# Kernel optimization log

Hardware: AMD Instinct MI355X
Metric: run time of the kernel (lower is better)

Reference implementation:

```python
import jax, jax.numpy as jnp
import numpy as np

E = 512    # len_embeddings
T = 32     # tokennum
H = 256    # hidden_unit
IT = 5     # ICI iterations
B = 4096   # batch
EPS = 1e-6


def setup_inputs() -> dict:
    key = jax.random.key(0)
    k0, k1, k2, k3, k4 = jax.random.split(key, 5)
    x = jax.random.normal(k0, (B, E), dtype=jnp.float32)
    glorot = np.sqrt(2.0 / (E + H)).astype(np.float32)
    w_in = jax.random.normal(k1, (T, E, H), dtype=jnp.float32) * glorot
    w_val = jax.random.normal(k2, (T, E, H), dtype=jnp.float32) * glorot
    # alphas: per-token, per-iteration inhibition strengths (trained; sample nonzero)
    alphas = jax.random.uniform(k3, (T, IT), dtype=jnp.float32) * 0.5
    # scales: per-token output scale (init 1.0, perturb slightly)
    scales = 1.0 + 0.1 * jax.random.normal(k4, (T, H), dtype=jnp.float32)
    gamma = jnp.ones((T, H), dtype=jnp.float32)
    beta = jnp.zeros((T, H), dtype=jnp.float32)
    return {"x": x, "w_in": w_in, "w_val": w_val, "alphas": alphas,
            "scales": scales, "gamma": gamma, "beta": beta}


def reference(x, w_in, w_val, alphas, scales, gamma, beta):
    # batched per-token projection: [B,E] x [T,E,H] -> [B,T,H]
    hidden = jnp.einsum('be,teh->bth', x, w_in)
    # iterative competitive inhibition (fixed small IT loop)
    x_t = jax.nn.relu(hidden)
    for i in range(alphas.shape[1]):
        m = jnp.mean(x_t, axis=-1, keepdims=True)          # [B,T,1]
        a = alphas[:, i][None, :, None]                     # [1,T,1]
        x_t = jax.nn.relu(x_t - a * m)
    sparse_g = scales[None] * x_t                           # [B,T,H]
    # gated value path
    value = jnp.einsum('be,teh->bth', x, w_val)
    s = sparse_g * value
    # per-token LayerNorm over hidden dim, eps=1e-6
    mu = jnp.mean(s, axis=-1, keepdims=True)
    var = jnp.mean((s - mu) ** 2, axis=-1, keepdims=True)
    out = (s - mu) / jnp.sqrt(var + EPS) * gamma[None] + beta[None]
    return out  # [B, T, H]
```

## Files before the change

### kernel.cpp

```cpp
#include <hip/hip_runtime.h>
#include <cstdint>

using u16 = unsigned short;
using u32 = unsigned int;

constexpr int kB  = 4096;
constexpr int kE  = 512;
constexpr int kT  = 32;
constexpr int kH  = 256;
constexpr int kIT = 5;
constexpr float kEPS = 1e-6f;

typedef __attribute__((ext_vector_type(8)))  short short8;
typedef __attribute__((ext_vector_type(16))) float floatx16;
typedef __attribute__((ext_vector_type(8)))  u16   ushort8;
typedef __attribute__((ext_vector_type(4)))  float floatv4;

__device__ __forceinline__ u16 f2bf(float f) {
  u32 u = __builtin_bit_cast(u32, f);
  return (u16)((u + 0x7fffu + ((u >> 16) & 1u)) >> 16);
}

__device__ __forceinline__ floatx16 mfma32(short8 a, short8 b, floatx16 c) {
  return __builtin_amdgcn_mfma_f32_32x32x16_bf16(a, b, c, 0, 0, 0);
}

__device__ __forceinline__ void ntstore4(float* p, float4 v) {
  __builtin_nontemporal_store(__builtin_bit_cast(floatv4, v), (floatv4*)p);
}

__global__ __launch_bounds__(256) void pack_x_kernel(
    const float* __restrict__ x, u16* __restrict__ xp) {
  __shared__ __attribute__((aligned(16))) float tile[64 * 132];
  const int slab = blockIdx.x >> 2;
  const int kg   = blockIdx.x & 3;
  const int tid  = threadIdx.x;

  const int r0 = tid >> 5;
  const int c0 = (tid & 31) * 4;
#pragma unroll
  for (int p = 0; p < 8; ++p) {
    const int r = p * 8 + r0;
    const float4 v = *(const float4*)(x + (size_t)(slab * 64 + r) * kE + kg * 128 + c0);
    *(float4*)(tile + r * 132 + c0) = v;
  }
  __syncthreads();

  const int wv = tid >> 6, lane = tid & 63;
#pragma unroll
  for (int q = 0; q < 4; ++q) {
    const int cc   = wv * 4 + q;
    const int ks_l = cc >> 1;
    const int mt   = cc & 1;
    const int rl   = mt * 32 + (lane & 31);
    const int kl   = ks_l * 16 + (lane >> 5) * 8;
    const float4 f0 = *(const float4*)(tile + rl * 132 + kl);
    const float4 f1 = *(const float4*)(tile + rl * 132 + kl + 4);
    ushort8 o;
    o[0] = f2bf(f0.x); o[1] = f2bf(f0.y); o[2] = f2bf(f0.z); o[3] = f2bf(f0.w);
    o[4] = f2bf(f1.x); o[5] = f2bf(f1.y); o[6] = f2bf(f1.z); o[7] = f2bf(f1.w);
    const int c = slab * 64 + (kg * 8 + ks_l) * 2 + mt;
    *(ushort8*)(xp + (size_t)c * 512 + lane * 8) = o;
  }
}

__global__ __launch_bounds__(256) void pack_w_kernel(
    const float* __restrict__ w_in, const float* __restrict__ w_val,
    u16* __restrict__ wp) {
  __shared__ __attribute__((aligned(16))) float tile[64 * 68];
  const int wb   = blockIdx.x;
  const int tl   = wb & 31;
  const int et   = tl >> 2;
  const int ht   = tl & 3;
  const int tm   = wb >> 5;
  const int t    = tm >> 1, mat = tm & 1;
  const int tid  = threadIdx.x;
  const float* src = (mat ? w_val : w_in) + (size_t)t * kE * kH +
                     (size_t)(et * 64) * kH + ht * 64;
  const int lrow = tid >> 4, lc4 = (tid & 15) * 4;
#pragma unroll
  for (int p = 0; p < 4; ++p) {
    const int e = lrow + p * 16;
    const float4 v = *(const float4*)(src + (size_t)e * kH + lc4);
    tile[e * 68 + lc4 + 0] = v.x; tile[e * 68 + lc4 + 1] = v.y;
    tile[e * 68 + lc4 + 2] = v.z; tile[e * 68 + lc4 + 3] = v.w;
  }
  __syncthreads();
  const int ks_l = tid >> 6, lane = tid & 63;
  const int kloc = ks_l * 16 + (lane >> 5) * 8;
#pragma unroll
  for (int nt_l = 0; nt_l < 2; ++nt_l) {
    const int nloc = nt_l * 32 + (lane & 31);
    ushort8 o;
#pragma unroll
    for (int j = 0; j < 8; ++j) o[j] = f2bf(tile[(kloc + j) * 68 + nloc]);
    const int c = t * 512 + (et * 4 + ks_l) * 16 + (ht * 2 + nt_l) * 2 + mat;
    *(ushort8*)(wp + (size_t)c * 512 + lane * 8) = o;
  }
}

__global__ __launch_bounds__(256, 2) void fused_kernel(
    const u16* __restrict__ xp, const u16* __restrict__ wp,
    const float* __restrict__ alphas, const float* __restrict__ scales,
    const float* __restrict__ gamma, const float* __restrict__ beta,
    float* __restrict__ out) {
  __shared__ __attribute__((aligned(16))) float sAcc[32 * 256];

  const int tid  = threadIdx.x;
  const int wv   = tid >> 6;
  const int lane = tid & 63;
  const int l31  = lane & 31;
  const int h    = lane >> 5;

  const int bid  = blockIdx.x;
  const int xcd  = bid & 7;
  const int r_   = bid >> 3;
  const int st   = r_ >> 6;
  const int wi   = r_ & 63;
  const int t    = xcd * 4 + (wi >> 4);
  const int slab = st * 16 + (wi & 15);

  const u16* xpb = xp + (size_t)slab * (32 * 2 * 512) + lane * 8;
  const u16* wpb = wp + (size_t)t * (32 * 16 * 512) + (size_t)(wv * 2) * 1024 + lane * 8;

  floatx16 ai[2][2], av[2][2];
#pragma unroll
  for (int m = 0; m < 2; ++m)
#pragma unroll
    for (int n = 0; n < 2; ++n) { ai[m][n] = (floatx16)0.f; av[m][n] = (floatx16)0.f; }

  short8 A[3][2], BI[3][2], BV[3][2];
#pragma unroll
  for (int p = 0; p < 2; ++p) {
    A[p][0]  = *(const short8*)(xpb + p * 1024);
    A[p][1]  = *(const short8*)(xpb + p * 1024 + 512);
    BI[p][0] = *(const short8*)(wpb + p * 8192);
    BV[p][0] = *(const short8*)(wpb + p * 8192 + 512);
    BI[p][1] = *(const short8*)(wpb + p * 8192 + 1024);
    BV[p][1] = *(const short8*)(wpb + p * 8192 + 1536);
  }

#pragma unroll
  for (int ks = 0; ks < 32; ++ks) {
    const int cur = ks % 3;
    const int nx  = (ks + 2) % 3;
    const int kn  = (ks < 30) ? ks + 2 : 31;
    A[nx][0]  = *(const short8*)(xpb + kn * 1024);
    A[nx][1]  = *(const short8*)(xpb + kn * 1024 + 512);
    BI[nx][0] = *(const short8*)(wpb + kn * 8192);
    BV[nx][0] = *(const short8*)(wpb + kn * 8192 + 512);
    BI[nx][1] = *(const short8*)(wpb + kn * 8192 + 1024);
    BV[nx][1] = *(const short8*)(wpb + kn * 8192 + 1536);
    ai[0][0] = mfma32(A[cur][0], BI[cur][0], ai[0][0]);
    ai[1][0] = mfma32(A[cur][1], BI[cur][0], ai[1][0]);
    ai[0][1] = mfma32(A[cur][0], BI[cur][1], ai[0][1]);
    ai[1][1] = mfma32(A[cur][1], BI[cur][1], ai[1][1]);
    av[0][0] = mfma32(A[cur][0], BV[cur][0], av[0][0]);
    av[1][0] = mfma32(A[cur][1], BV[cur][0], av[1][0]);
    av[0][1] = mfma32(A[cur][0], BV[cur][1], av[0][1]);
    av[1][1] = mfma32(A[cur][1], BV[cur][1], av[1][1]);
  }

  const float inv_h = 1.0f / kH;
  float al[kIT];
#pragma unroll
  for (int i = 0; i < kIT; ++i) al[i] = alphas[t * kIT + i] * inv_h;

  const int row_r = tid >> 3;
  const int seg   = tid & 7;
  const int r4    = (row_r & 7) << 2;

#pragma unroll
  for (int mt = 0; mt < 2; ++mt) {
    __syncthreads();
#pragma unroll
    for (int nt = 0; nt < 2; ++nt)
#pragma unroll
      for (int q = 0; q < 16; ++q) {
        const int r   = (q & 3) + 8 * (q >> 2) + 4 * h;
        const int col = wv * 64 + nt * 32 + l31;
        sAcc[r * 256 + (col ^ ((r & 7) << 2))] = ai[mt][nt][q];
      }
    __syncthreads();

    float4 xt[8];
#pragma unroll
    for (int j = 0; j < 8; ++j) {
      xt[j] = *(const float4*)(sAcc + row_r * 256 + seg * 32 + ((4 * j) ^ r4));
#pragma unroll
      for (int i = 0; i < 4; ++i) xt[j][i] = fmaxf(xt[j][i], 0.f);
    }

#pragma unroll
    for (int it = 0; it < kIT; ++it) {
      float4 s4 = xt[0];
#pragma unroll
      for (int j = 1; j < 8; ++j) s4 += xt[j];
      float v = s4.x + s4.y + s4.z + s4.w;
      v += __shfl_xor(v, 1, 8);
      v += __shfl_xor(v, 2, 8);
      v += __shfl_xor(v, 4, 8);
      const float m = al[it] * v;
#pragma unroll
      for (int j = 0; j < 8; ++j)
#pragma unroll
        for (int i = 0; i < 4; ++i) xt[j][i] = fmaxf(xt[j][i] - m, 0.f);
    }

    __syncthreads();
#pragma unroll
    for (int nt = 0; nt < 2; ++nt)
#pragma unroll
      for (int q = 0; q < 16; ++q) {
        const int r   = (q & 3) + 8 * (q >> 2) + 4 * h;
        const int col = wv * 64 + nt * 32 + l31;
        sAcc[r * 256 + (col ^ ((r & 7) << 2))] = av[mt][nt][q];
      }
    __syncthreads();

    float4 res[8];
    float sum = 0.f, ssq = 0.f;
#pragma unroll
    for (int j = 0; j < 8; ++j) {
      const int cb = seg * 32 + ((4 * j) ^ r4);
      const int lc = seg * 32 + 4 * j;
      const float4 a4 = *(const float4*)(sAcc + row_r * 256 + cb);
      const float4 sc = *(const float4*)(scales + t * kH + lc);
      float4 s;
#pragma unroll
      for (int i = 0; i < 4; ++i) {
        s[i] = sc[i] * xt[j][i] * a4[i];
        sum += s[i];
        ssq += s[i] * s[i];
      }
      res[j] = s;
    }
    sum += __shfl_xor(sum, 1, 8);  ssq += __shfl_xor(ssq, 1, 8);
    sum += __shfl_xor(sum, 2, 8);  ssq += __shfl_xor(ssq, 2, 8);
    sum += __shfl_xor(sum, 4, 8);  ssq += __shfl_xor(ssq, 4, 8);
    const float mu  = sum * inv_h;
    const float var = ssq * inv_h - mu * mu;
    const float rs  = rsqrtf(var + kEPS);

#pragma unroll
    for (int j = 0; j < 8; ++j) {
      const int cb = seg * 32 + ((4 * j) ^ r4);
      const int lc = seg * 32 + 4 * j;
      const float4 g4 = *(const float4*)(gamma + t * kH + lc);
      const float4 b4 = *(const float4*)(beta + t * kH + lc);
      float4 o;
#pragma unroll
      for (int i = 0; i < 4; ++i) o[i] = (res[j][i] - mu) * rs * g4[i] + b4[i];
      *(float4*)(sAcc + row_r * 256 + cb) = o;
    }
    __syncthreads();

#pragma unroll
    for (int r8 = 0; r8 < 8; ++r8) {
      const int rr = wv * 8 + r8;
      const int rb = (rr & 7) << 2;
      const float4 v = *(const float4*)(sAcc + rr * 256 + ((4 * lane) ^ rb));
      ntstore4(out + (size_t)(slab * 64 + mt * 32 + rr) * (kT * kH) + t * kH + 4 * lane, v);
    }
  }
}

extern "C" void kernel_launch(void* const* d_in, const int* in_sizes, int n_in,
                              void* d_out, int out_size, void* d_ws, size_t ws_size,
                              hipStream_t stream) {
  const float* x      = (const float*)d_in[0];
  const float* w_in   = (const float*)d_in[1];
  const float* w_val  = (const float*)d_in[2];
  const float* alphas = (const float*)d_in[3];
  const float* scales = (const float*)d_in[4];
  const float* gamma  = (const float*)d_in[5];
  const float* beta   = (const float*)d_in[6];
  float* out = (float*)d_out;

  u16* xp = (u16*)d_ws;
  u16* wp = xp + (size_t)64 * 32 * 2 * 512;

  pack_x_kernel<<<256, 256, 0, stream>>>(x, xp);
  pack_w_kernel<<<2048, 256, 0, stream>>>(w_in, w_val, wp);
  fused_kernel<<<kT * (kB / 64), 256, 0, stream>>>(xp, wp, alphas, scales,
                                                   gamma, beta, out);
}
```

Before: 346.6 us.

## Stage weight tiles through LDS with async global_load_lds double buffering

Replaces the per-wave direct global register loads of the packed weight fragments with asynchronous global-to-LDS copies. The copies are double-buffered across 16 K-steps of two sub-steps each, and each step ends in a block barrier. Each wave copies a quarter of the tile and all waves then read their fragments from LDS, while x fragments stay in registers and are double-buffered. This aims to cut per-wave global load latency and register-pipelined vector loads. In exchange it adds LDS traffic, 16 barriers, and reuses the accumulator smem region as the weight buffer.

```diff
diff --git a/kernel.cpp b/kernel.cpp
--- a/kernel.cpp
+++ b/kernel.cpp
@@ -27,6 +27,12 @@
 
 __device__ __forceinline__ void ntstore4(float* p, float4 v) {
   __builtin_nontemporal_store(__builtin_bit_cast(floatv4, v), (floatv4*)p);
+}
+
+__device__ __forceinline__ void gload16(const u16* gsrc, u16* ldst) {
+  __builtin_amdgcn_global_load_lds(
+      (const __attribute__((address_space(1))) u32*)gsrc,
+      (__attribute__((address_space(3))) u32*)ldst, 16, 0, 0);
 }
 
 __global__ __launch_bounds__(256) void pack_x_kernel(
@@ -104,7 +110,8 @@
     const float* __restrict__ alphas, const float* __restrict__ scales,
     const float* __restrict__ gamma, const float* __restrict__ beta,
     float* __restrict__ out) {
-  __shared__ __attribute__((aligned(16))) float sAcc[32 * 256];
+  __shared__ __attribute__((aligned(16))) u16 sB[2][16384];
+  float* sAcc = (float*)sB;
 
   const int tid  = threadIdx.x;
   const int wv   = tid >> 6;
@@ -121,7 +128,9 @@
   const int slab = st * 16 + (wi & 15);
 
   const u16* xpb = xp + (size_t)slab * (32 * 2 * 512) + lane * 8;
-  const u16* wpb = wp + (size_t)t * (32 * 16 * 512) + (size_t)(wv * 2) * 1024 + lane * 8;
+  const u16* wpt = wp + (size_t)t * (32 * 16 * 512);
+  const u16* wps = wpt + lane * 8;
+  const int  q0  = wv * 8;
 
   floatx16 ai[2][2], av[2][2];
 #pragma unroll
@@ -129,36 +138,52 @@
 #pragma unroll
     for (int n = 0; n < 2; ++n) { ai[m][n] = (floatx16)0.f; av[m][n] = (floatx16)0.f; }
 
-  short8 A[3][2], BI[3][2], BV[3][2];
-#pragma unroll
-  for (int p = 0; p < 2; ++p) {
-    A[p][0]  = *(const short8*)(xpb + p * 1024);
-    A[p][1]  = *(const short8*)(xpb + p * 1024 + 512);
-    BI[p][0] = *(const short8*)(wpb + p * 8192);
-    BV[p][0] = *(const short8*)(wpb + p * 8192 + 512);
-    BI[p][1] = *(const short8*)(wpb + p * 8192 + 1024);
-    BV[p][1] = *(const short8*)(wpb + p * 8192 + 1536);
-  }
-
-#pragma unroll
-  for (int ks = 0; ks < 32; ++ks) {
-    const int cur = ks % 3;
-    const int nx  = (ks + 2) % 3;
-    const int kn  = (ks < 30) ? ks + 2 : 31;
-    A[nx][0]  = *(const short8*)(xpb + kn * 1024);
-    A[nx][1]  = *(const short8*)(xpb + kn * 1024 + 512);
-    BI[nx][0] = *(const short8*)(wpb + kn * 8192);
-    BV[nx][0] = *(const short8*)(wpb + kn * 8192 + 512);
-    BI[nx][1] = *(const short8*)(wpb + kn * 8192 + 1024);
-    BV[nx][1] = *(const short8*)(wpb + kn * 8192 + 1536);
-    ai[0][0] = mfma32(A[cur][0], BI[cur][0], ai[0][0]);
-    ai[1][0] = mfma32(A[cur][1], BI[cur][0], ai[1][0]);
-    ai[0][1] = mfma32(A[cur][0], BI[cur][1], ai[0][1]);
-    ai[1][1] = mfma32(A[cur][1], BI[cur][1], ai[1][1]);
-    av[0][0] = mfma32(A[cur][0], BV[cur][0], av[0][0]);
-    av[1][0] = mfma32(A[cur][1], BV[cur][0], av[1][0]);
-    av[0][1] = mfma32(A[cur][0], BV[cur][1], av[0][1]);
-    av[1][1] = mfma32(A[cur][1], BV[cur][1], av[1][1]);
+  short8 A_[2][2][2];
+
+#pragma unroll
+  for (int j = 0; j < 8; ++j) {
+    const int q = q0 + j;
+    gload16(wps + (size_t)q * 512, (u16*)sB[0] + q * 512);
+  }
+#pragma unroll
+  for (int ksl = 0; ksl < 2; ++ksl)
+#pragma unroll
+    for (int m = 0; m < 2; ++m)
+      A_[0][ksl][m] = *(const short8*)(xpb + (ksl * 2 + m) * 512);
+  __syncthreads();
+
+#pragma unroll
+  for (int p = 0; p < 16; ++p) {
+    const int db = p & 1, nx = db ^ 1;
+    if (p < 15) {
+#pragma unroll
+      for (int j = 0; j < 8; ++j) {
+        const int q = q0 + j;
+        gload16(wps + (size_t)((p + 1) * 32 + q) * 512, (u16*)sB[nx] + q * 512);
+      }
+#pragma unroll
+      for (int ksl = 0; ksl < 2; ++ksl)
+#pragma unroll
+        for (int m = 0; m < 2; ++m)
+          A_[nx][ksl][m] = *(const short8*)(xpb + (((p + 1) * 2 + ksl) * 2 + m) * 512);
+    }
+    const u16* sBp = (const u16*)sB[db] + lane * 8;
+#pragma unroll
+    for (int ksl = 0; ksl < 2; ++ksl) {
+      const short8 BI0 = *(const short8*)(sBp + (ksl * 16 + (wv * 2 + 0) * 2 + 0) * 512);
+      const short8 BV0 = *(const short8*)(sBp + (ksl * 16 + (wv * 2 + 0) * 2 + 1) * 512);
+      const short8 BI1 = *(const short8*)(sBp + (ksl * 16 + (wv * 2 + 1) * 2 + 0) * 512);
+      const short8 BV1 = *(const short8*)(sBp + (ksl * 16 + (wv * 2 + 1) * 2 + 1) * 512);
+      ai[0][0] = mfma32(A_[db][ksl][0], BI0, ai[0][0]);
+      ai[1][0] = mfma32(A_[db][ksl][1], BI0, ai[1][0]);
+      ai[0][1] = mfma32(A_[db][ksl][0], BI1, ai[0][1]);
+      ai[1][1] = mfma32(A_[db][ksl][1], BI1, ai[1][1]);
+      av[0][0] = mfma32(A_[db][ksl][0], BV0, av[0][0]);
+      av[1][0] = mfma32(A_[db][ksl][1], BV0, av[1][0]);
+      av[0][1] = mfma32(A_[db][ksl][0], BV1, av[0][1]);
+      av[1][1] = mfma32(A_[db][ksl][1], BV1, av[1][1]);
+    }
+    __syncthreads();
   }
 
   const float inv_h = 1.0f / kH;
```

Result: faster. 315.8 us (-8.9%).

## Stream GEMM operands through per-wave LDS ring via global_load_lds

Applied to the files above, without the earlier changes.

The main K loop now loads A and B fragments straight into a per-wave three-slot LDS ring with direct-to-LDS global loads instead of holding a triple-buffered register pipeline. Each step waits on vmcnt, reads the fragments back from LDS, and raises wave priority around the MFMA group. This is meant to cut register pressure and keep more global loads in flight. The cost is an extra LDS round trip per step and hand-written waitcnt logic that must match the load count exactly. The LDS buffer is also reused as the epilogue accumulator scratch.

```diff
diff --git a/kernel.cpp b/kernel.cpp
--- a/kernel.cpp
+++ b/kernel.cpp
@@ -27,6 +27,12 @@
 
 __device__ __forceinline__ void ntstore4(float* p, float4 v) {
   __builtin_nontemporal_store(__builtin_bit_cast(floatv4, v), (floatv4*)p);
+}
+
+__device__ __forceinline__ void gload16(const u16* gsrc, u16* ldst) {
+  __builtin_amdgcn_global_load_lds(
+      (const __attribute__((address_space(1))) u32*)gsrc,
+      (__attribute__((address_space(3))) u32*)ldst, 16, 0, 0);
 }
 
 __global__ __launch_bounds__(256) void pack_x_kernel(
@@ -104,7 +110,8 @@
     const float* __restrict__ alphas, const float* __restrict__ scales,
     const float* __restrict__ gamma, const float* __restrict__ beta,
     float* __restrict__ out) {
-  __shared__ __attribute__((aligned(16))) float sAcc[32 * 256];
+  __shared__ __attribute__((aligned(16))) u16 ring[4][3][3072];
+  float* sAcc = (float*)ring;
 
   const int tid  = threadIdx.x;
   const int wv   = tid >> 6;
@@ -120,8 +127,9 @@
   const int t    = xcd * 4 + (wi >> 4);
   const int slab = st * 16 + (wi & 15);
 
-  const u16* xpb = xp + (size_t)slab * (32 * 2 * 512) + lane * 8;
-  const u16* wpb = wp + (size_t)t * (32 * 16 * 512) + (size_t)(wv * 2) * 1024 + lane * 8;
+  const u16* xsrc = xp + (size_t)slab * (32 * 2 * 512) + lane * 8;
+  const u16* bsrc = wp + (size_t)t * (32 * 16 * 512) + (wv * 4) * 512 + lane * 8;
+  u16* const ring_w = &ring[wv][0][0];
 
   floatx16 ai[2][2], av[2][2];
 #pragma unroll
@@ -129,36 +137,48 @@
 #pragma unroll
     for (int n = 0; n < 2; ++n) { ai[m][n] = (floatx16)0.f; av[m][n] = (floatx16)0.f; }
 
-  short8 A[3][2], BI[3][2], BV[3][2];
-#pragma unroll
-  for (int p = 0; p < 2; ++p) {
-    A[p][0]  = *(const short8*)(xpb + p * 1024);
-    A[p][1]  = *(const short8*)(xpb + p * 1024 + 512);
-    BI[p][0] = *(const short8*)(wpb + p * 8192);
-    BV[p][0] = *(const short8*)(wpb + p * 8192 + 512);
-    BI[p][1] = *(const short8*)(wpb + p * 8192 + 1024);
-    BV[p][1] = *(const short8*)(wpb + p * 8192 + 1536);
-  }
-
-#pragma unroll
-  for (int ks = 0; ks < 32; ++ks) {
-    const int cur = ks % 3;
-    const int nx  = (ks + 2) % 3;
-    const int kn  = (ks < 30) ? ks + 2 : 31;
-    A[nx][0]  = *(const short8*)(xpb + kn * 1024);
-    A[nx][1]  = *(const short8*)(xpb + kn * 1024 + 512);
-    BI[nx][0] = *(const short8*)(wpb + kn * 8192);
-    BV[nx][0] = *(const short8*)(wpb + kn * 8192 + 512);
-    BI[nx][1] = *(const short8*)(wpb + kn * 8192 + 1024);
-    BV[nx][1] = *(const short8*)(wpb + kn * 8192 + 1536);
-    ai[0][0] = mfma32(A[cur][0], BI[cur][0], ai[0][0]);
-    ai[1][0] = mfma32(A[cur][1], BI[cur][0], ai[1][0]);
-    ai[0][1] = mfma32(A[cur][0], BI[cur][1], ai[0][1]);
-    ai[1][1] = mfma32(A[cur][1], BI[cur][1], ai[1][1]);
-    av[0][0] = mfma32(A[cur][0], BV[cur][0], av[0][0]);
-    av[1][0] = mfma32(A[cur][1], BV[cur][0], av[1][0]);
-    av[0][1] = mfma32(A[cur][0], BV[cur][1], av[0][1]);
-    av[1][1] = mfma32(A[cur][1], BV[cur][1], av[1][1]);
+  auto issue = [&](int pb, int slot) {
+    u16* d = ring_w + slot * 3072;
+    const u16* a = xsrc + (size_t)pb * 1024;
+    const u16* b = bsrc + (size_t)pb * 8192;
+    gload16(a,        d);
+    gload16(a + 512,  d + 512);
+    gload16(b,        d + 1024);
+    gload16(b + 512,  d + 1536);
+    gload16(b + 1024, d + 2048);
+    gload16(b + 1536, d + 2560);
+  };
+
+  issue(0, 0);
+  issue(1, 1);
+
+#pragma unroll
+  for (int p = 0; p < 32; ++p) {
+    if (p < 31) { asm volatile("s_waitcnt vmcnt(6)" ::: "memory"); }
+    else        { asm volatile("s_waitcnt vmcnt(0)" ::: "memory"); }
+    __builtin_amdgcn_sched_barrier(0);
+    if (p < 30) issue(p + 2, (p + 2) % 3);
+
+    const u16* base = ring_w + (p % 3) * 3072 + lane * 8;
+    const short8 A0  = *(const short8*)(base);
+    const short8 A1  = *(const short8*)(base + 512);
+    const short8 BI0 = *(const short8*)(base + 1024);
+    const short8 BV0 = *(const short8*)(base + 1536);
+    const short8 BI1 = *(const short8*)(base + 2048);
+    const short8 BV1 = *(const short8*)(base + 2560);
+    asm volatile("s_waitcnt lgkmcnt(0)" ::: "memory");
+    __builtin_amdgcn_sched_barrier(0);
+
+    __builtin_amdgcn_s_setprio(1);
+    ai[0][0] = mfma32(A0, BI0, ai[0][0]);
+    ai[1][0] = mfma32(A1, BI0, ai[1][0]);
+    ai[0][1] = mfma32(A0, BI1, ai[0][1]);
+    ai[1][1] = mfma32(A1, BI1, ai[1][1]);
+    av[0][0] = mfma32(A0, BV0, av[0][0]);
+    av[1][0] = mfma32(A1, BV0, av[1][0]);
+    av[0][1] = mfma32(A0, BV1, av[0][1]);
+    av[1][1] = mfma32(A1, BV1, av[1][1]);
+    __builtin_amdgcn_s_setprio(0);
   }
 
   const float inv_h = 1.0f / kH;
```

Result: faster. 302.4 us (-12.7%).

## Split fused kernel across 8 waves with one N-tile each to raise occupancy

Applied to the files above, without the earlier changes.

The fused GEMM+inhibition+LayerNorm kernel now launches 512 threads per block. Each of the 8 waves owns one 32-column N tile instead of two, which halves the accumulator and operand registers per wave, and prefetch depth drops from a 3-stage to a 2-stage register ring. The epilogue is remapped so 16 threads share a row, with wider shuffle reductions. The intent is higher occupancy and latency hiding through more resident waves. In exchange, each wave reuses fewer A fragments, so global loads per MFMA rise and block-level synchronisation costs more.

```diff
diff --git a/kernel.cpp b/kernel.cpp
--- a/kernel.cpp
+++ b/kernel.cpp
@@ -99,7 +99,7 @@
   }
 }
 
-__global__ __launch_bounds__(256, 2) void fused_kernel(
+__global__ __launch_bounds__(512, 4) void fused_kernel(
     const u16* __restrict__ xp, const u16* __restrict__ wp,
     const float* __restrict__ alphas, const float* __restrict__ scales,
     const float* __restrict__ gamma, const float* __restrict__ beta,
@@ -120,45 +120,35 @@
   const int t    = xcd * 4 + (wi >> 4);
   const int slab = st * 16 + (wi & 15);
 
-  const u16* xpb = xp + (size_t)slab * (32 * 2 * 512) + lane * 8;
-  const u16* wpb = wp + (size_t)t * (32 * 16 * 512) + (size_t)(wv * 2) * 1024 + lane * 8;
-
-  floatx16 ai[2][2], av[2][2];
-#pragma unroll
-  for (int m = 0; m < 2; ++m)
-#pragma unroll
-    for (int n = 0; n < 2; ++n) { ai[m][n] = (floatx16)0.f; av[m][n] = (floatx16)0.f; }
-
-  short8 A[3][2], BI[3][2], BV[3][2];
-#pragma unroll
-  for (int p = 0; p < 2; ++p) {
-    A[p][0]  = *(const short8*)(xpb + p * 1024);
-    A[p][1]  = *(const short8*)(xpb + p * 1024 + 512);
-    BI[p][0] = *(const short8*)(wpb + p * 8192);
-    BV[p][0] = *(const short8*)(wpb + p * 8192 + 512);
-    BI[p][1] = *(const short8*)(wpb + p * 8192 + 1024);
-    BV[p][1] = *(const short8*)(wpb + p * 8192 + 1536);
-  }
-
-#pragma unroll
-  for (int ks = 0; ks < 32; ++ks) {
-    const int cur = ks % 3;
-    const int nx  = (ks + 2) % 3;
-    const int kn  = (ks < 30) ? ks + 2 : 31;
-    A[nx][0]  = *(const short8*)(xpb + kn * 1024);
-    A[nx][1]  = *(const short8*)(xpb + kn * 1024 + 512);
-    BI[nx][0] = *(const short8*)(wpb + kn * 8192);
-    BV[nx][0] = *(const short8*)(wpb + kn * 8192 + 512);
-    BI[nx][1] = *(const short8*)(wpb + kn * 8192 + 1024);
-    BV[nx][1] = *(const short8*)(wpb + kn * 8192 + 1536);
-    ai[0][0] = mfma32(A[cur][0], BI[cur][0], ai[0][0]);
-    ai[1][0] = mfma32(A[cur][1], BI[cur][0], ai[1][0]);
-    ai[0][1] = mfma32(A[cur][0], BI[cur][1], ai[0][1]);
-    ai[1][1] = mfma32(A[cur][1], BI[cur][1], ai[1][1]);
-    av[0][0] = mfma32(A[cur][0], BV[cur][0], av[0][0]);
-    av[1][0] = mfma32(A[cur][1], BV[cur][0], av[1][0]);
-    av[0][1] = mfma32(A[cur][0], BV[cur][1], av[0][1]);
-    av[1][1] = mfma32(A[cur][1], BV[cur][1], av[1][1]);
+  const u16* xsrc = xp + (size_t)slab * (32 * 2 * 512) + lane * 8;
+  const u16* bsrc = wp + (size_t)t * (32 * 16 * 512) + (size_t)(wv * 2) * 512 + lane * 8;
+
+  floatx16 ai[2], av[2];
+#pragma unroll
+  for (int m = 0; m < 2; ++m) { ai[m] = (floatx16)0.f; av[m] = (floatx16)0.f; }
+
+  short8 A0[2], A1[2], BI[2], BV[2];
+#pragma unroll
+  for (int pb = 0; pb < 2; ++pb) {
+    A0[pb] = *(const short8*)(xsrc + pb * 1024);
+    A1[pb] = *(const short8*)(xsrc + pb * 1024 + 512);
+    BI[pb] = *(const short8*)(bsrc + (size_t)pb * 8192);
+    BV[pb] = *(const short8*)(bsrc + (size_t)pb * 8192 + 512);
+  }
+
+#pragma unroll
+  for (int p = 0; p < 32; ++p) {
+    const int cur = p & 1;
+    ai[0] = mfma32(A0[cur], BI[cur], ai[0]);
+    ai[1] = mfma32(A1[cur], BI[cur], ai[1]);
+    av[0] = mfma32(A0[cur], BV[cur], av[0]);
+    av[1] = mfma32(A1[cur], BV[cur], av[1]);
+    if (p < 30) {
+      A0[cur] = *(const short8*)(xsrc + (p + 2) * 1024);
+      A1[cur] = *(const short8*)(xsrc + (p + 2) * 1024 + 512);
+      BI[cur] = *(const short8*)(bsrc + (size_t)(p + 2) * 8192);
+      BV[cur] = *(const short8*)(bsrc + (size_t)(p + 2) * 8192 + 512);
+    }
   }
 
   const float inv_h = 1.0f / kH;
@@ -166,27 +156,25 @@
 #pragma unroll
   for (int i = 0; i < kIT; ++i) al[i] = alphas[t * kIT + i] * inv_h;
 
-  const int row_r = tid >> 3;
-  const int seg   = tid & 7;
+  const int row_r = tid >> 4;
+  const int seg   = tid & 15;
   const int r4    = (row_r & 7) << 2;
 
 #pragma unroll
   for (int mt = 0; mt < 2; ++mt) {
     __syncthreads();
 #pragma unroll
-    for (int nt = 0; nt < 2; ++nt)
-#pragma unroll
-      for (int q = 0; q < 16; ++q) {
-        const int r   = (q & 3) + 8 * (q >> 2) + 4 * h;
-        const int col = wv * 64 + nt * 32 + l31;
-        sAcc[r * 256 + (col ^ ((r & 7) << 2))] = ai[mt][nt][q];
-      }
-    __syncthreads();
-
-    float4 xt[8];
-#pragma unroll
-    for (int j = 0; j < 8; ++j) {
-      xt[j] = *(const float4*)(sAcc + row_r * 256 + seg * 32 + ((4 * j) ^ r4));
+    for (int q = 0; q < 16; ++q) {
+      const int r   = (q & 3) + 8 * (q >> 2) + 4 * h;
+      const int col = wv * 32 + l31;
+      sAcc[r * 256 + (col ^ ((r & 7) << 2))] = ai[mt][q];
+    }
+    __syncthreads();
+
+    float4 xt[4];
+#pragma unroll
+    for (int j = 0; j < 4; ++j) {
+      xt[j] = *(const float4*)(sAcc + row_r * 256 + ((seg * 16 + 4 * j) ^ r4));
 #pragma unroll
       for (int i = 0; i < 4; ++i) xt[j][i] = fmaxf(xt[j][i], 0.f);
     }
@@ -195,35 +183,34 @@
     for (int it = 0; it < kIT; ++it) {
       float4 s4 = xt[0];
 #pragma unroll
-      for (int j = 1; j < 8; ++j) s4 += xt[j];
+      for (int j = 1; j < 4; ++j) s4 += xt[j];
       float v = s4.x + s4.y + s4.z + s4.w;
-      v += __shfl_xor(v, 1, 8);
-      v += __shfl_xor(v, 2, 8);
-      v += __shfl_xor(v, 4, 8);
+      v += __shfl_xor(v, 1, 16);
+      v += __shfl_xor(v, 2, 16);
+      v += __shfl_xor(v, 4, 16);
+      v += __shfl_xor(v, 8, 16);
       const float m = al[it] * v;
 #pragma unroll
-      for (int j = 0; j < 8; ++j)
+      for (int j = 0; j < 4; ++j)
 #pragma unroll
         for (int i = 0; i < 4; ++i) xt[j][i] = fmaxf(xt[j][i] - m, 0.f);
     }
 
     __syncthreads();
 #pragma unroll
-    for (int nt = 0; nt < 2; ++nt)
-#pragma unroll
-      for (int q = 0; q < 16; ++q) {
-        const int r   = (q & 3) + 8 * (q >> 2) + 4 * h;
-        const int col = wv * 64 + nt * 32 + l31;
-        sAcc[r * 256 + (col ^ ((r & 7) << 2))] = av[mt][nt][q];
-      }
-    __syncthreads();
-
-    float4 res[8];
+    for (int q = 0; q < 16; ++q) {
+      const int r   = (q & 3) + 8 * (q >> 2) + 4 * h;
+      const int col = wv * 32 + l31;
+      sAcc[r * 256 + (col ^ ((r & 7) << 2))] = av[mt][q];
+    }
+    __syncthreads();
+
+    float4 res[4];
     float sum = 0.f, ssq = 0.f;
 #pragma unroll
-    for (int j = 0; j < 8; ++j) {
-      const int cb = seg * 32 + ((4 * j) ^ r4);
-      const int lc = seg * 32 + 4 * j;
+    for (int j = 0; j < 4; ++j) {
+      const int lc = seg * 16 + 4 * j;
+      const int cb = lc ^ r4;
       const float4 a4 = *(const float4*)(sAcc + row_r * 256 + cb);
       const float4 sc = *(const float4*)(scales + t * kH + lc);
       float4 s;
@@ -235,17 +222,18 @@
       }
       res[j] = s;
     }
-    sum += __shfl_xor(sum, 1, 8);  ssq += __shfl_xor(ssq, 1, 8);
-    sum += __shfl_xor(sum, 2, 8);  ssq += __shfl_xor(ssq, 2, 8);
-    sum += __shfl_xor(sum, 4, 8);  ssq += __shfl_xor(ssq, 4, 8);
+    sum += __shfl_xor(sum, 1, 16);  ssq += __shfl_xor(ssq, 1, 16);
+    sum += __shfl_xor(sum, 2, 16);  ssq += __shfl_xor(ssq, 2, 16);
+    sum += __shfl_xor(sum, 4, 16);  ssq += __shfl_xor(ssq, 4, 16);
+    sum += __shfl_xor(sum, 8, 16);  ssq += __shfl_xor(ssq, 8, 16);
     const float mu  = sum * inv_h;
     const float var = ssq * inv_h - mu * mu;
     const float rs  = rsqrtf(var + kEPS);
 
 #pragma unroll
-    for (int j = 0; j < 8; ++j) {
-      const int cb = seg * 32 + ((4 * j) ^ r4);
-      const int lc = seg * 32 + 4 * j;
+    for (int j = 0; j < 4; ++j) {
+      const int lc = seg * 16 + 4 * j;
+      const int cb = lc ^ r4;
       const float4 g4 = *(const float4*)(gamma + t * kH + lc);
       const float4 b4 = *(const float4*)(beta + t * kH + lc);
       float4 o;
@@ -256,8 +244,8 @@
     __syncthreads();
 
 #pragma unroll
-    for (int r8 = 0; r8 < 8; ++r8) {
-      const int rr = wv * 8 + r8;
+    for (int r8 = 0; r8 < 4; ++r8) {
+      const int rr = wv * 4 + r8;
       const int rb = (rr & 7) << 2;
       const float4 v = *(const float4*)(sAcc + rr * 256 + ((4 * lane) ^ rb));
       ntstore4(out + (size_t)(slab * 64 + mt * 32 + rr) * (kT * kH) + t * kH + 4 * lane, v);
@@ -282,6 +270,6 @@
 
   pack_x_kernel<<<256, 256, 0, stream>>>(x, xp);
   pack_w_kernel<<<2048, 256, 0, stream>>>(w_in, w_val, wp);
-  fused_kernel<<<kT * (kB / 64), 256, 0, stream>>>(xp, wp, alphas, scales,
+  fused_kernel<<<kT * (kB / 64), 512, 0, stream>>>(xp, wp, alphas, scales,
                                                    gamma, beta, out);
 }
```

New measurement: 290.2 us. -16.3%, faster.
